# Kernel optimization log

Hardware: AMD Instinct MI355X
Metric: run time of the kernel (lower is better)

## Reference

```python
import jax, jax.numpy as jnp
import numpy as np

B, T, D = 32, 576, 1024          # T = (384//16)**2 patches
H, G, HD = 16, 4, 64             # num_heads, query_groups, head_dim
BASE = 10000.0
SCALE = 1.0 / float(np.sqrt(HD))


def _rope2d(x):
    # x: [B, T, nH, HD]; 2D rotary: split head_dim into 4 groups of freq_dim.
    b, t, nh, hd = x.shape
    fd = hd // 4
    grid = int(np.sqrt(t))
    inv_freq = 1.0 / (BASE ** (jnp.arange(fd, dtype=jnp.float32) / fd))  # [fd]
    pos = jnp.arange(grid, dtype=jnp.float32)
    gx, gy = jnp.meshgrid(pos, pos, indexing='ij')          # [grid, grid]
    theta_x = gx.reshape(-1)[:, None] * inv_freq            # [T, fd]
    theta_y = gy.reshape(-1)[:, None] * inv_freq            # [T, fd]
    sx = jnp.sin(theta_x)[None, :, None, :]                 # [1, T, 1, fd]
    cx = jnp.cos(theta_x)[None, :, None, :]
    sy = jnp.sin(theta_y)[None, :, None, :]
    cy = jnp.cos(theta_y)[None, :, None, :]
    xr = x.reshape(b, t, nh, 4, fd)
    x1, x2, y1, y2 = xr[..., 0, :], xr[..., 1, :], xr[..., 2, :], xr[..., 3, :]
    out = jnp.stack([x1 * cx - x2 * sx,
                     x1 * sx + x2 * cx,
                     y1 * cy - y2 * sy,
                     y1 * sy + y2 * cy], axis=-2)           # [B, T, nH, 4, fd]
    return out.reshape(b, t, nh, hd)


def setup_inputs() -> dict:
    key = jax.random.key(0)
    k1, k2, k3 = jax.random.split(key, 3)
    x = jax.random.normal(k1, (B, T, D), dtype=jnp.float32)
    w_qkv = jax.random.normal(k2, (H * HD + 2 * G * HD, D), dtype=jnp.float32) * 0.02
    w_o = jax.random.normal(k3, (D, H * HD), dtype=jnp.float32) * 0.02
    return {"x": x, "w_qkv": w_qkv, "w_o": w_o, "window_size": -1}


def reference(x, w_qkv, w_o, window_size):
    # window_size=-1 -> full (non-windowed) attention, matching SDPA fallback.
    b, t, _ = x.shape
    qkv = x @ w_qkv.T                                       # [B, T, H*HD + 2*G*HD]
    q, k, v = jnp.split(qkv, [H * HD, H * HD + G * HD], axis=-1)
    q = q.reshape(b, t, H, HD)
    k = k.reshape(b, t, G, HD)
    v = v.reshape(b, t, G, HD)
    q = _rope2d(q)
    k = _rope2d(k)
    q = q.transpose(0, 2, 1, 3)                             # [B, H, T, HD]
    k = k.transpose(0, 2, 1, 3)                             # [B, G, T, HD]
    v = v.transpose(0, 2, 1, 3)
    hpg = H // G
    k = jnp.repeat(k, hpg, axis=1)                          # [B, H, T, HD]
    v = jnp.repeat(v, hpg, axis=1)
    scores = jnp.einsum('bhqd,bhkd->bhqk', q, k) * SCALE    # [B, H, T, T]
    attn = jax.nn.softmax(scores, axis=-1)
    out = jnp.einsum('bhqk,bhkd->bhqd', attn, v)            # [B, H, T, HD]
    out = out.transpose(0, 2, 1, 3).reshape(b, t, H * HD)
    return out @ w_o.T                                      # [B, T, D]
```

## Files before the change

kernel.cpp:

```cpp
#include <hip/hip_runtime.h>

typedef unsigned short u16;
typedef unsigned long long u64;
typedef __attribute__((ext_vector_type(8))) short short8;
typedef __attribute__((ext_vector_type(4))) float f32x4;

#define B_ 32
#define T_ 576
#define H_ 16
#define G_ 4
#define HD_ 64
#define DM 1024
#define NQKV 1536
#define BT (B_*T_)
#define GRID2D 24
#define FD 16

__device__ __forceinline__ u16 f2bf(float f) {
  unsigned u = __float_as_uint(f);
  u = (u + 0x7FFFu + ((u >> 16) & 1u)) >> 16;
  return (u16)u;
}
__device__ __forceinline__ float exp2v(float x) {
  float r;
  asm("v_exp_f32 %0, %1" : "=v"(r) : "v"(x));
  return r;
}

__device__ __forceinline__ void gl_lds16(const u16* g, u16* lds) {
  __builtin_amdgcn_global_load_lds((const __attribute__((address_space(1))) unsigned int*)g,
                                   (__attribute__((address_space(3))) unsigned int*)lds, 16, 0, 0);
}

__global__ __launch_bounds__(256) void cvt_kernel(const float4* __restrict__ in, u16* __restrict__ o, int n4) {
  int i = blockIdx.x * 256 + threadIdx.x;
  if (i >= n4) return;
  float4 v = in[i];
  u64 pk = (u64)f2bf(v.x) | ((u64)f2bf(v.y) << 16) | ((u64)f2bf(v.z) << 32) | ((u64)f2bf(v.w) << 48);
  *(u64*)(o + (size_t)i * 4) = pk;
}

__global__ __launch_bounds__(256) void rope_table_kernel(float4* __restrict__ tab) {
  int i = blockIdx.x * 256 + threadIdx.x;
  if (i >= T_ * FD) return;
  int t = i >> 4, j = i & 15;
  float inv = powf(10000.0f, -(float)j / 16.0f);
  float tx = (float)(t / GRID2D) * inv;
  float ty = (float)(t % GRID2D) * inv;
  float4 r;
  r.x = sinf(tx); r.y = cosf(tx); r.z = sinf(ty); r.w = cosf(ty);
  tab[i] = r;
}

__device__ __forceinline__ void stage_ab(const u16* __restrict__ A, const u16* __restrict__ Bw,
                                         int m0, int n0, int k0, u16* Asb, u16* Bsb,
                                         int w, int srow, int skk) {
#pragma unroll
  for (int ii = 0; ii < 2; ++ii) {
    int i = w * 2 + ii;
    int row = i * 16 + srow;
    gl_lds16(A + (size_t)(m0 + row) * DM + k0 + skk, Asb + i * 512);
    gl_lds16(Bw + (size_t)(n0 + row) * DM + k0 + skk, Bsb + i * 512);
  }
}

template <int EPI, int NX>
__global__ __launch_bounds__(256) void gemm_nt(const u16* __restrict__ A, const u16* __restrict__ Bw,
                                               u16* __restrict__ o0, u16* __restrict__ o1,
                                               u16* __restrict__ o2, float* __restrict__ fo,
                                               const float4* __restrict__ tab) {
  __shared__ __align__(16) u16 As[2][128 * 32];
  __shared__ __align__(16) u16 Bs[2][128 * 32];
  const int tid = threadIdx.x;
  const int w = tid >> 6, l = tid & 63;
  const int wm = w >> 1, wn = w & 1;
  const int L = blockIdx.y * NX + blockIdx.x;
  const int cpx = (NX * 144) / 8;
  const int W = (L & 7) * cpx + (L >> 3);
  const int by = W / NX, bx = W - by * NX;
  const int m0 = by * 128, n0 = bx * 128;
  const int lr = l & 15, lg = l >> 4;
  const int srow = l >> 2;
  const int skk = (l & 3) * 8;
  f32x4 acc[4][4] = {};

  stage_ab(A, Bw, m0, n0, 0, &As[0][0], &Bs[0][0], w, srow, skk);
  asm volatile("s_waitcnt vmcnt(0)\n\ts_barrier" ::: "memory");

  int cur = 0;
  for (int kt = 0; kt < 31; ++kt) {
    stage_ab(A, Bw, m0, n0, (kt + 1) * 32, &As[cur ^ 1][0], &Bs[cur ^ 1][0], w, srow, skk);
    short8 af[4], bfr[4];
#pragma unroll
    for (int mi = 0; mi < 4; ++mi)
      af[mi] = *(const short8*)(&As[cur][(wm * 64 + mi * 16 + lr) * 32 + lg * 8]);
#pragma unroll
    for (int ni = 0; ni < 4; ++ni)
      bfr[ni] = *(const short8*)(&Bs[cur][(wn * 64 + ni * 16 + lr) * 32 + lg * 8]);
    __builtin_amdgcn_s_setprio(1);
#pragma unroll
    for (int mi = 0; mi < 4; ++mi)
#pragma unroll
      for (int ni = 0; ni < 4; ++ni)
        acc[mi][ni] = __builtin_amdgcn_mfma_f32_16x16x32_bf16(af[mi], bfr[ni], acc[mi][ni], 0, 0, 0);
    __builtin_amdgcn_s_setprio(0);
    asm volatile("s_waitcnt vmcnt(0)\n\ts_barrier" ::: "memory");
    cur ^= 1;
  }
  {
    short8 af[4], bfr[4];
#pragma unroll
    for (int mi = 0; mi < 4; ++mi)
      af[mi] = *(const short8*)(&As[cur][(wm * 64 + mi * 16 + lr) * 32 + lg * 8]);
#pragma unroll
    for (int ni = 0; ni < 4; ++ni)
      bfr[ni] = *(const short8*)(&Bs[cur][(wn * 64 + ni * 16 + lr) * 32 + lg * 8]);
#pragma unroll
    for (int mi = 0; mi < 4; ++mi)
#pragma unroll
      for (int ni = 0; ni < 4; ++ni)
        acc[mi][ni] = __builtin_amdgcn_mfma_f32_16x16x32_bf16(af[mi], bfr[ni], acc[mi][ni], 0, 0, 0);
  }

  if (EPI == 0) {
    const float qs = 0.125f * 1.44269504f;
    const int nbase = n0 + wn * 64;
#pragma unroll
    for (int mi = 0; mi < 4; ++mi) {
#pragma unroll
      for (int r = 0; r < 4; ++r) {
        int mg = m0 + wm * 64 + mi * 16 + lg * 4 + r;
        int bb = mg / T_, t = mg - bb * T_;
        float v0 = acc[mi][0][r], v1 = acc[mi][1][r], v2 = acc[mi][2][r], v3 = acc[mi][3][r];
        if (nbase < 1280) {
          float4 tb = tab[t * FD + lr];
          float sc = (nbase < 1024) ? qs : 1.0f;
          float e0 = (v0 * tb.y - v1 * tb.x) * sc;
          float e1 = (v0 * tb.x + v1 * tb.y) * sc;
          float e2 = (v2 * tb.w - v3 * tb.z) * sc;
          float e3 = (v2 * tb.z + v3 * tb.w) * sc;
          u16* dst;
          if (nbase < 1024) {
            int h = nbase >> 6;
            dst = o0 + (((size_t)bb * H_ + h) * T_ + t) * 64 + lr;
          } else {
            int g = (nbase - 1024) >> 6;
            dst = o1 + (((size_t)bb * G_ + g) * T_ + t) * 64 + lr;
          }
          dst[0] = f2bf(e0); dst[16] = f2bf(e1); dst[32] = f2bf(e2); dst[48] = f2bf(e3);
        } else {
          int g = (nbase - 1280) >> 6;
          u16* dst = o2 + ((size_t)bb * G_ + g) * (64 * (size_t)T_) + t;
          dst[(0 * 16 + lr) * (size_t)T_] = f2bf(v0);
          dst[(1 * 16 + lr) * (size_t)T_] = f2bf(v1);
          dst[(2 * 16 + lr) * (size_t)T_] = f2bf(v2);
          dst[(3 * 16 + lr) * (size_t)T_] = f2bf(v3);
        }
      }
    }
  } else {
#pragma unroll
    for (int mi = 0; mi < 4; ++mi)
#pragma unroll
      for (int ni = 0; ni < 4; ++ni)
#pragma unroll
        for (int r = 0; r < 4; ++r) {
          int mg = m0 + wm * 64 + mi * 16 + lg * 4 + r;
          int ng = n0 + wn * 64 + ni * 16 + lr;
          fo[(size_t)mg * 1024 + ng] = acc[mi][ni][r];
        }
  }
}

__device__ __forceinline__ void stage_kv(const u16* __restrict__ k, const u16* __restrict__ vt,
                                         size_t kvbase, int kt, u16* Ksb, u16* Vsb,
                                         int w, int srow, int sblk) {
#pragma unroll
  for (int ii = 0; ii < 2; ++ii) {
    int i = w * 2 + ii;
    int row = i * 8 + srow;
    gl_lds16(k + kvbase + (size_t)(kt * 64 + row) * 64 + sblk * 8, Ksb + i * 512);
    gl_lds16(vt + kvbase + (size_t)row * T_ + kt * 64 + sblk * 8, Vsb + i * 512);
  }
}

__global__ __launch_bounds__(256) void attn_kernel(const u16* __restrict__ q, const u16* __restrict__ k,
                                                   const u16* __restrict__ vt, u16* __restrict__ o) {
  __shared__ __align__(16) u16 Ks[2][64 * 64];
  __shared__ __align__(16) u16 Vs[2][64 * 64];
  __shared__ __align__(16) u16 Pl[4][16 * 72];
  int L = blockIdx.x;
  int W = (L & 7) * 576 + (L >> 3);
  int qt = W % 9;
  int bh = W / 9;
  int h = bh & 15, b = bh >> 4;
  int g = h >> 2;
  int tid = threadIdx.x;
  int w = tid >> 6, l = tid & 63;
  int lr = l & 15, lg = l >> 4;
  const size_t kvbase = ((size_t)(b * G_ + g)) * (T_ * 64);

  const u16* qptr = q + (((size_t)(b * H_ + h)) * T_ + qt * 64 + w * 16 + lr) * 64;
  short8 qf0 = *(const short8*)(qptr + lg * 8);
  short8 qf1 = *(const short8*)(qptr + 32 + lg * 8);

  float ls[4] = {0.f, 0.f, 0.f, 0.f};
  f32x4 oacc[4];
#pragma unroll
  for (int dt = 0; dt < 4; ++dt) oacc[dt] = (f32x4){0.f, 0.f, 0.f, 0.f};

  const int srow = l >> 3;
  const int sblk = (l & 7) ^ (srow & 7);

  stage_kv(k, vt, kvbase, 0, &Ks[0][0], &Vs[0][0], w, srow, sblk);
  asm volatile("s_waitcnt vmcnt(0)\n\ts_barrier" ::: "memory");

  int cur = 0;
  for (int kt = 0; kt < 9; ++kt) {
    if (kt < 8)
      stage_kv(k, vt, kvbase, kt + 1, &Ks[cur ^ 1][0], &Vs[cur ^ 1][0], w, srow, sblk);

    f32x4 sacc[4];
#pragma unroll
    for (int ct = 0; ct < 4; ++ct) {
      sacc[ct] = (f32x4){0.f, 0.f, 0.f, 0.f};
      int row = ct * 16 + lr;
      int i0 = (0 * 4 + lg) ^ (row & 7);
      int i1 = (1 * 4 + lg) ^ (row & 7);
      short8 kf0 = *(const short8*)(&Ks[cur][row * 64 + i0 * 8]);
      short8 kf1 = *(const short8*)(&Ks[cur][row * 64 + i1 * 8]);
      sacc[ct] = __builtin_amdgcn_mfma_f32_16x16x32_bf16(qf0, kf0, sacc[ct], 0, 0, 0);
      sacc[ct] = __builtin_amdgcn_mfma_f32_16x16x32_bf16(qf1, kf1, sacc[ct], 0, 0, 0);
    }

    float p[4][4];
#pragma unroll
    for (int ct = 0; ct < 4; ++ct)
#pragma unroll
      for (int r = 0; r < 4; ++r) p[ct][r] = exp2v(sacc[ct][r]);
#pragma unroll
    for (int r = 0; r < 4; ++r) ls[r] += (p[0][r] + p[1][r]) + (p[2][r] + p[3][r]);

    u16* pl = &Pl[w][0];
#pragma unroll
    for (int ct = 0; ct < 4; ++ct)
#pragma unroll
      for (int r = 0; r < 4; ++r)
        pl[(lg * 4 + r) * 72 + ct * 16 + lr] = (u16)((__float_as_uint(p[ct][r]) + 0x8000u) >> 16);
    asm volatile("s_waitcnt lgkmcnt(0)" ::: "memory");
#pragma unroll
    for (int c = 0; c < 2; ++c) {
      short8 pf = *(const short8*)(pl + lr * 72 + c * 32 + lg * 8);
#pragma unroll
      for (int dt = 0; dt < 4; ++dt) {
        int row = dt * 16 + lr;
        int blk = (c * 4 + lg) ^ (row & 7);
        short8 vf = *(const short8*)(&Vs[cur][row * 64 + blk * 8]);
        oacc[dt] = __builtin_amdgcn_mfma_f32_16x16x32_bf16(pf, vf, oacc[dt], 0, 0, 0);
      }
    }

    if (kt < 8) {
      asm volatile("s_waitcnt vmcnt(0)\n\ts_barrier" ::: "memory");
      cur ^= 1;
    }
  }

#pragma unroll
  for (int mk = 1; mk <= 8; mk <<= 1)
#pragma unroll
    for (int r = 0; r < 4; ++r) ls[r] += __shfl_xor(ls[r], mk);

#pragma unroll
  for (int dt = 0; dt < 4; ++dt)
#pragma unroll
    for (int r = 0; r < 4; ++r) {
      int trow = qt * 64 + w * 16 + lg * 4 + r;
      float v = oacc[dt][r] / ls[r];
      o[((size_t)b * T_ + trow) * 1024 + h * 64 + dt * 16 + lr] = f2bf(v);
    }
}

extern "C" void kernel_launch(void* const* d_in, const int* in_sizes, int n_in,
                              void* d_out, int out_size, void* d_ws, size_t ws_size,
                              hipStream_t stream) {
  const float* x = (const float*)d_in[0];
  const float* wqkv = (const float*)d_in[1];
  const float* wo = (const float*)d_in[2];
  float* out = (float*)d_out;

  u16* ws = (u16*)d_ws;
  u16* xb = ws;
  u16* wqkvb = xb + (size_t)BT * DM;
  u16* wob = wqkvb + (size_t)NQKV * DM;
  u16* qb = wob + (size_t)DM * DM;
  u16* kb = qb + (size_t)BT * DM;
  u16* vtb = kb + (size_t)B_ * G_ * T_ * 64;
  float4* tab = (float4*)(vtb + (size_t)B_ * G_ * T_ * 64);
  u16* ob = xb;

  cvt_kernel<<<(BT * DM / 4 + 255) / 256, 256, 0, stream>>>((const float4*)x, xb, BT * DM / 4);
  cvt_kernel<<<(NQKV * DM / 4 + 255) / 256, 256, 0, stream>>>((const float4*)wqkv, wqkvb, NQKV * DM / 4);
  cvt_kernel<<<(DM * DM / 4 + 255) / 256, 256, 0, stream>>>((const float4*)wo, wob, DM * DM / 4);
  rope_table_kernel<<<(T_ * FD + 255) / 256, 256, 0, stream>>>(tab);
  gemm_nt<0, 12><<<dim3(12, 144), 256, 0, stream>>>(xb, wqkvb, qb, kb, vtb, nullptr, tab);
  attn_kernel<<<B_ * H_ * 9, 256, 0, stream>>>(qb, kb, vtb, ob);
  gemm_nt<1, 8><<<dim3(8, 144), 256, 0, stream>>>(ob, wob, nullptr, nullptr, nullptr, out, nullptr);
}
```

Measured before the change: 293.4 us.

## Deepen GEMM LDS pipeline to four stages with partial vmcnt waits

The GEMM main loop moves from double buffering to a four-buffer ring with three tiles prefetched ahead. Each iteration waits only until older loads have landed (vmcnt(8)) rather than draining all outstanding loads, so more global-to-LDS traffic stays in flight during MFMA work. Sched barriers stop the compiler from moving code across the wait. The cost is twice the LDS per block (64 KB), which may lower occupancy, and the vmcnt counts depend on stage_ab issuing exactly four loads per thread.

```diff
diff --git a/kernel.cpp b/kernel.cpp
--- a/kernel.cpp
+++ b/kernel.cpp
@@ -64,13 +64,18 @@
   }
 }
 
+#define WAITBAR(N)                                        \
+  __builtin_amdgcn_sched_barrier(0);                      \
+  asm volatile("s_waitcnt vmcnt(" #N ")\n\ts_barrier" ::: "memory"); \
+  __builtin_amdgcn_sched_barrier(0);
+
 template <int EPI, int NX>
 __global__ __launch_bounds__(256) void gemm_nt(const u16* __restrict__ A, const u16* __restrict__ Bw,
                                                u16* __restrict__ o0, u16* __restrict__ o1,
                                                u16* __restrict__ o2, float* __restrict__ fo,
                                                const float4* __restrict__ tab) {
-  __shared__ __align__(16) u16 As[2][128 * 32];
-  __shared__ __align__(16) u16 Bs[2][128 * 32];
+  __shared__ __align__(16) u16 As[4][128 * 32];
+  __shared__ __align__(16) u16 Bs[4][128 * 32];
   const int tid = threadIdx.x;
   const int w = tid >> 6, l = tid & 63;
   const int wm = w >> 1, wn = w & 1;
@@ -84,43 +89,37 @@
   const int skk = (l & 3) * 8;
   f32x4 acc[4][4] = {};
 
-  stage_ab(A, Bw, m0, n0, 0, &As[0][0], &Bs[0][0], w, srow, skk);
-  asm volatile("s_waitcnt vmcnt(0)\n\ts_barrier" ::: "memory");
-
-  int cur = 0;
-  for (int kt = 0; kt < 31; ++kt) {
-    stage_ab(A, Bw, m0, n0, (kt + 1) * 32, &As[cur ^ 1][0], &Bs[cur ^ 1][0], w, srow, skk);
-    short8 af[4], bfr[4];
-#pragma unroll
-    for (int mi = 0; mi < 4; ++mi)
-      af[mi] = *(const short8*)(&As[cur][(wm * 64 + mi * 16 + lr) * 32 + lg * 8]);
-#pragma unroll
-    for (int ni = 0; ni < 4; ++ni)
-      bfr[ni] = *(const short8*)(&Bs[cur][(wn * 64 + ni * 16 + lr) * 32 + lg * 8]);
-    __builtin_amdgcn_s_setprio(1);
-#pragma unroll
-    for (int mi = 0; mi < 4; ++mi)
-#pragma unroll
-      for (int ni = 0; ni < 4; ++ni)
-        acc[mi][ni] = __builtin_amdgcn_mfma_f32_16x16x32_bf16(af[mi], bfr[ni], acc[mi][ni], 0, 0, 0);
-    __builtin_amdgcn_s_setprio(0);
-    asm volatile("s_waitcnt vmcnt(0)\n\ts_barrier" ::: "memory");
-    cur ^= 1;
-  }
-  {
-    short8 af[4], bfr[4];
-#pragma unroll
-    for (int mi = 0; mi < 4; ++mi)
-      af[mi] = *(const short8*)(&As[cur][(wm * 64 + mi * 16 + lr) * 32 + lg * 8]);
-#pragma unroll
-    for (int ni = 0; ni < 4; ++ni)
-      bfr[ni] = *(const short8*)(&Bs[cur][(wn * 64 + ni * 16 + lr) * 32 + lg * 8]);
-#pragma unroll
-    for (int mi = 0; mi < 4; ++mi)
-#pragma unroll
-      for (int ni = 0; ni < 4; ++ni)
-        acc[mi][ni] = __builtin_amdgcn_mfma_f32_16x16x32_bf16(af[mi], bfr[ni], acc[mi][ni], 0, 0, 0);
-  }
+#define COMPUTE(buf)                                                                        \
+  {                                                                                         \
+    short8 af[4], bfr[4];                                                                   \
+    _Pragma("unroll") for (int mi = 0; mi < 4; ++mi)                                        \
+        af[mi] = *(const short8*)(&As[buf][(wm * 64 + mi * 16 + lr) * 32 + lg * 8]);        \
+    _Pragma("unroll") for (int ni = 0; ni < 4; ++ni)                                        \
+        bfr[ni] = *(const short8*)(&Bs[buf][(wn * 64 + ni * 16 + lr) * 32 + lg * 8]);       \
+    __builtin_amdgcn_s_setprio(1);                                                          \
+    _Pragma("unroll") for (int mi = 0; mi < 4; ++mi)                                        \
+        _Pragma("unroll") for (int ni = 0; ni < 4; ++ni)                                    \
+            acc[mi][ni] = __builtin_amdgcn_mfma_f32_16x16x32_bf16(af[mi], bfr[ni],          \
+                                                                  acc[mi][ni], 0, 0, 0);    \
+    __builtin_amdgcn_s_setprio(0);                                                          \
+  }
+
+  stage_ab(A, Bw, m0, n0, 0,  &As[0][0], &Bs[0][0], w, srow, skk);
+  stage_ab(A, Bw, m0, n0, 32, &As[1][0], &Bs[1][0], w, srow, skk);
+  stage_ab(A, Bw, m0, n0, 64, &As[2][0], &Bs[2][0], w, srow, skk);
+  WAITBAR(8)
+
+  for (int t = 0; t < 29; ++t) {
+    stage_ab(A, Bw, m0, n0, (t + 3) * 32, &As[(t + 3) & 3][0], &Bs[(t + 3) & 3][0], w, srow, skk);
+    COMPUTE(t & 3);
+    WAITBAR(8)
+  }
+  COMPUTE(1);
+  WAITBAR(4)
+  COMPUTE(2);
+  WAITBAR(0)
+  COMPUTE(3);
+#undef COMPUTE
 
   if (EPI == 0) {
     const float qs = 0.125f * 1.44269504f;
```

Result: slower. 317.3 us (+8.1%).
